# Kernel tuning notes

Measured on AMD Instinct MI355X. Metric: run time of the kernel, lower is better.

## Reference

```python
import math
import jax, jax.numpy as jnp
import numpy as np

B, Q, HID = 4, 4, 4096
NH, NKV, HD = 32, 8, 128
GROUPS = NH // NKV
CACHE_LEN = 4096
CACHE_MAX = CACHE_LEN + 512  # prefill_len + max_len(512)
ROPE_THETA = 500000.0
SCALE = 1.0 / math.sqrt(128.0)  # hardcoded softmax_scale in module


def rotate_half(x):
    x1, x2 = jnp.split(x, 2, axis=-1)
    return jnp.concatenate([-x2, x1], axis=-1)


def setup_inputs() -> dict:
    key = jax.random.key(0)
    ks = jax.random.split(key, 8)
    std = 0.02
    # RoPE angles for positions [CACHE_LEN, CACHE_LEN+Q)
    pos = (CACHE_LEN + jnp.arange(Q)).astype(jnp.float32)
    inv_freq = 1.0 / (ROPE_THETA ** (jnp.arange(0, HD, 2, dtype=jnp.float32) / HD))
    freqs = pos[:, None] * inv_freq[None, :]            # [Q, HD/2]
    emb = jnp.concatenate([freqs, freqs], axis=-1)      # [Q, HD]
    cos = jnp.broadcast_to(jnp.cos(emb)[None], (B, Q, HD)).astype(jnp.float32)
    sin = jnp.broadcast_to(jnp.sin(emb)[None], (B, Q, HD)).astype(jnp.float32)
    return {
        "hidden_states": jax.random.normal(ks[0], (B, Q, HID), jnp.float32),
        "cos": cos,
        "sin": sin,
        "K_Cache": jax.random.normal(ks[1], (B, NKV, CACHE_MAX, HD), jnp.float32) * 0.5,
        "V_Cache": jax.random.normal(ks[2], (B, NKV, CACHE_MAX, HD), jnp.float32) * 0.5,
        "Wq": jax.random.normal(ks[3], (NH * HD, HID), jnp.float32) * std,
        "Wk": jax.random.normal(ks[4], (NKV * HD, HID), jnp.float32) * std,
        "Wv": jax.random.normal(ks[5], (NKV * HD, HID), jnp.float32) * std,
        "Wo": jax.random.normal(ks[6], (HID, NH * HD), jnp.float32) * std,
        "cache_lens": int(CACHE_LEN),
    }


def reference(hidden_states, cos, sin, K_Cache, V_Cache, Wq, Wk, Wv, Wo, cache_lens):
    b, q, _ = hidden_states.shape
    # projections (torch Linear: x @ W.T), reshape to [b, h, q, d]
    qs = jnp.einsum('bsh,oh->bso', hidden_states, Wq).reshape(b, q, NH, HD).transpose(0, 2, 1, 3)
    ks = jnp.einsum('bsh,oh->bso', hidden_states, Wk).reshape(b, q, NKV, HD).transpose(0, 2, 1, 3)
    vs = jnp.einsum('bsh,oh->bso', hidden_states, Wv).reshape(b, q, NKV, HD).transpose(0, 2, 1, 3)
    # RoPE, unsqueeze_dim=1 (head axis)
    c, s = cos[:, None, :, :], sin[:, None, :, :]
    qs = qs * c + rotate_half(qs) * s
    ks = ks * c + rotate_half(ks) * s
    # scatter new K/V into the cache at offset cache_lens
    K_Cache = K_Cache.at[:, :, cache_lens:cache_lens + q, :].set(ks)
    V_Cache = V_Cache.at[:, :, cache_lens:cache_lens + q, :].set(vs)
    # K_total/V_total = cache prefix ++ fresh keys/values; GQA repeat
    K_total = jnp.repeat(jnp.concatenate([K_Cache[:, :, :cache_lens, :], ks], axis=2), GROUPS, axis=1)
    V_total = jnp.repeat(jnp.concatenate([V_Cache[:, :, :cache_lens, :], vs], axis=2), GROUPS, axis=1)
    scores = jnp.einsum('bhqd,bhkd->bhqk', qs, K_total) * SCALE
    # causal mask over the appended q tokens, cache prefix fully visible
    tri = jnp.triu(jnp.ones((q, q), bool), 1)
    mask = jnp.concatenate([jnp.zeros((q, cache_lens), bool), tri], axis=1)
    scores = jnp.where(mask[None, None], -jnp.inf, scores)
    attn = jax.nn.softmax(scores.astype(jnp.float32), axis=-1).astype(V_total.dtype)
    out = jnp.einsum('bhqk,bhkd->bhqd', attn, V_total)
    out = out.transpose(0, 2, 1, 3).reshape(b, q, NH * HD)
    return jnp.einsum('bsh,oh->bso', out, Wo)
```

## Files before the change

### kernel.cpp

```cpp
#include <hip/hip_runtime.h>
#include <hip/hip_fp16.h>
#include <math.h>

#define HIDK 4096
#define NHQ 32
#define HD 128
#define CMAX 4608
#define CLEN 4096
#define NCH 32
#define SCALE 0.08838834764831845f

__device__ __forceinline__ float4 ld4(const float* p) { return *reinterpret_cast<const float4*>(p); }
__device__ __forceinline__ float dot4(float4 a, float4 b) { return a.x*b.x + a.y*b.y + a.z*b.z + a.w*b.w; }

__global__ __launch_bounds__(256) void gemm3_kernel(
    const float* __restrict__ X,
    const float* __restrict__ W1, const float* __restrict__ W2, const float* __restrict__ W3,
    int n1, int n2,
    float* __restrict__ o1, int os1,
    float* __restrict__ o2, int os2,
    float* __restrict__ o3, int os3)
{
  __shared__ float Xs[2][16][256];

  const int tid = threadIdx.x, lane = tid & 63, w = tid >> 6;
  const int o = blockIdx.x * 8 + w * 2;

  const float* Wb; float* ob; int os;
  if (o < n1)           { Wb = W1 + (size_t)o * HIDK;            ob = o1 + o;            os = os1; }
  else if (o < n1 + n2) { const int f = o - n1;      Wb = W2 + (size_t)f * HIDK; ob = o2 + f; os = os2; }
  else                  { const int f = o - n1 - n2; Wb = W3 + (size_t)f * HIDK; ob = o3 + f; os = os3; }

  const int strow = tid >> 6;
  const int stcol = (tid & 63) * 4;

  float acc0[16], acc1[16];
  #pragma unroll
  for (int b = 0; b < 16; ++b) { acc0[b] = 0.f; acc1[b] = 0.f; }

  #pragma unroll
  for (int j = 0; j < 4; ++j)
    *(float4*)&Xs[0][strow + j * 4][stcol] = ld4(X + (size_t)(strow + j * 4) * HIDK + stcol);

  int cur = 0;
  #pragma unroll 2
  for (int kt = 0; kt < 16; ++kt) {
    const float4 w0 = ld4(Wb + (size_t)kt * 256 + lane * 4);
    const float4 w1 = ld4(Wb + HIDK + (size_t)kt * 256 + lane * 4);
    float4 g[4];
    if (kt < 15) {
      #pragma unroll
      for (int j = 0; j < 4; ++j)
        g[j] = ld4(X + (size_t)(strow + j * 4) * HIDK + (kt + 1) * 256 + stcol);
    }
    __syncthreads();
    #pragma unroll
    for (int b = 0; b < 16; ++b) {
      const float4 x4 = *(const float4*)&Xs[cur][b][lane * 4];
      acc0[b] += dot4(x4, w0);
      acc1[b] += dot4(x4, w1);
    }
    if (kt < 15) {
      #pragma unroll
      for (int j = 0; j < 4; ++j)
        *(float4*)&Xs[cur ^ 1][strow + j * 4][stcol] = g[j];
    }
    cur ^= 1;
  }

  #pragma unroll
  for (int m = 1; m < 64; m <<= 1)
    #pragma unroll
    for (int b = 0; b < 16; ++b) {
      acc0[b] += __shfl_xor(acc0[b], m, 64);
      acc1[b] += __shfl_xor(acc1[b], m, 64);
    }
  if (lane == 0) {
    #pragma unroll
    for (int b = 0; b < 16; ++b) {
      ob[(size_t)b * os]     = acc0[b];
      ob[(size_t)b * os + 1] = acc1[b];
    }
  }
}

__global__ __launch_bounds__(256) void qt_prep_kernel(
    const float* __restrict__ qraw, const float* __restrict__ cosp,
    const float* __restrict__ sinp, float* __restrict__ qt)
{
  const int e = blockIdx.x * 256 + threadIdx.x;
  const int r = e & 15;
  const int d = (e >> 4) & 127;
  const int bkv = e >> 11;
  const int b = bkv >> 3, kv = bkv & 7;
  const int s = r & 3, hl = r >> 2;
  const float* qp = qraw + (size_t)(b * 4 + s) * HIDK + (kv * 4 + hl) * HD;
  const float c  = cosp[(b * 4 + s) * HD + d];
  const float sn = sinp[(b * 4 + s) * HD + d];
  const float sgn = (d < 64) ? -1.f : 1.f;
  qt[e] = (qp[d] * c + sgn * qp[d ^ 64] * sn) * SCALE;
}

__global__ __launch_bounds__(128) void attn3_kernel(
    const float* __restrict__ qt, const float* __restrict__ Kc, const float* __restrict__ Vc,
    __half* __restrict__ partOh, float* __restrict__ partM, float* __restrict__ partL)
{
  __shared__ float Plds[2][16][66];
  __shared__ float Oex[16][132];
  __shared__ float MLe[32];

  const int tid = threadIdx.x, lane = tid & 63, w = tid >> 6;
  const int chunk = blockIdx.x & 31, bkv = blockIdx.x >> 5;
  const int b = bkv >> 3, kv = bkv & 7;
  const int p0 = chunk * 128 + w * 64;

  const float* qtb = qt + (size_t)bkv * 2048;
  const float* Kp  = Kc + ((size_t)bkv * CMAX + p0 + lane) * HD;

  float sc[16];
  #pragma unroll
  for (int r = 0; r < 16; ++r) sc[r] = 0.f;
  #pragma unroll 4
  for (int d4 = 0; d4 < 32; ++d4) {
    const float4 k4 = ld4(Kp + d4 * 4);
    #pragma unroll
    for (int r = 0; r < 16; ++r) sc[r] += k4.x * qtb[(d4 * 4 + 0) * 16 + r];
    #pragma unroll
    for (int r = 0; r < 16; ++r) sc[r] += k4.y * qtb[(d4 * 4 + 1) * 16 + r];
    #pragma unroll
    for (int r = 0; r < 16; ++r) sc[r] += k4.z * qtb[(d4 * 4 + 2) * 16 + r];
    #pragma unroll
    for (int r = 0; r < 16; ++r) sc[r] += k4.w * qtb[(d4 * 4 + 3) * 16 + r];
  }

  float m[16], l[16];
  #pragma unroll
  for (int r = 0; r < 16; ++r) {
    float mx = sc[r];
    #pragma unroll
    for (int st = 1; st < 64; st <<= 1) mx = fmaxf(mx, __shfl_xor(mx, st, 64));
    const float p = __expf(sc[r] - mx);
    float ls = p;
    #pragma unroll
    for (int st = 1; st < 64; st <<= 1) ls += __shfl_xor(ls, st, 64);
    m[r] = mx; l[r] = ls;
    Plds[w][r][lane] = p;
  }

  const int dsub = lane & 31, par = lane >> 5;
  const float* Vp = Vc + ((size_t)bkv * CMAX + p0 + par) * HD + dsub * 4;
  float4 o[16];
  #pragma unroll
  for (int r = 0; r < 16; ++r) o[r] = make_float4(0.f, 0.f, 0.f, 0.f);
  #pragma unroll 4
  for (int i = 0; i < 32; ++i) {
    const float4 v4 = ld4(Vp + (size_t)(2 * i) * HD);
    #pragma unroll
    for (int r = 0; r < 16; ++r) {
      const float p = Plds[w][r][2 * i + par];
      o[r].x += p * v4.x; o[r].y += p * v4.y; o[r].z += p * v4.z; o[r].w += p * v4.w;
    }
  }
  #pragma unroll
  for (int r = 0; r < 16; ++r) {
    o[r].x += __shfl_xor(o[r].x, 32, 64);
    o[r].y += __shfl_xor(o[r].y, 32, 64);
    o[r].z += __shfl_xor(o[r].z, 32, 64);
    o[r].w += __shfl_xor(o[r].w, 32, 64);
  }

  if (w == 1) {
    if (lane < 32) {
      #pragma unroll
      for (int r = 0; r < 16; ++r) *(float4*)&Oex[r][dsub * 4] = o[r];
    }
    if (lane == 0) {
      #pragma unroll
      for (int r = 0; r < 16; ++r) { MLe[r] = m[r]; MLe[16 + r] = l[r]; }
    }
  }
  __syncthreads();
  if (w == 0 && lane < 32) {
    #pragma unroll
    for (int r = 0; r < 16; ++r) {
      const float m1 = MLe[r], l1 = MLe[16 + r];
      const float M  = fmaxf(m[r], m1);
      const float a0 = __expf(m[r] - M), a1 = __expf(m1 - M);
      const float4 o1 = *(const float4*)&Oex[r][dsub * 4];
      const float ox = a0 * o[r].x + a1 * o1.x;
      const float oy = a0 * o[r].y + a1 * o1.y;
      const float oz = a0 * o[r].z + a1 * o1.z;
      const float ow = a0 * o[r].w + a1 * o1.w;
      const int row = (b * NHQ + kv * 4 + (r >> 2)) * 4 + (r & 3);
      const size_t idx = ((size_t)row * NCH + chunk) * HD + dsub * 4;
      *(__half2*)&partOh[idx]     = __floats2half2_rn(ox, oy);
      *(__half2*)&partOh[idx + 2] = __floats2half2_rn(oz, ow);
      if (dsub == 0) {
        partM[row * NCH + chunk] = M;
        partL[row * NCH + chunk] = a0 * l[r] + a1 * l1;
      }
    }
  }
}

__global__ __launch_bounds__(64) void combine_kernel(
    const float* __restrict__ qt, const float* __restrict__ kraw, const float* __restrict__ vraw,
    const float* __restrict__ cosp, const float* __restrict__ sinp,
    const __half* __restrict__ partOh, const float* __restrict__ partM, const float* __restrict__ partL,
    float* __restrict__ attn)
{
  const int bid = blockIdx.x;
  const int s = bid & 3;
  const int h = (bid >> 2) & 31;
  const int b = bid >> 7;
  const int kv = h >> 2;
  const int lane = threadIdx.x;
  const int d0 = lane * 2;

  float M = -INFINITY;
  #pragma unroll 4
  for (int c = 0; c < NCH; ++c) M = fmaxf(M, partM[bid * NCH + c]);

  const int rloc = (h & 3) * 4 + s;
  const float qr0 = qt[((size_t)(b * 8 + kv) * 128 + d0) * 16 + rloc];
  const float qr1 = qt[((size_t)(b * 8 + kv) * 128 + d0 + 1) * 16 + rloc];

  float sj[4] = {0.f, 0.f, 0.f, 0.f};
  float Mp = M;
  #pragma unroll
  for (int j = 0; j < 4; ++j) {
    if (j <= s) {
      const float* kp = kraw + (size_t)(b * 4 + j) * 1024 + kv * HD;
      const float c0 = cosp[(b * 4 + j) * HD + d0],     sn0 = sinp[(b * 4 + j) * HD + d0];
      const float c1 = cosp[(b * 4 + j) * HD + d0 + 1], sn1 = sinp[(b * 4 + j) * HD + d0 + 1];
      const float sg0 = (d0 < 64) ? -1.f : 1.f;
      const float sg1 = ((d0 + 1) < 64) ? -1.f : 1.f;
      const float kr0 = kp[d0] * c0 + sg0 * kp[d0 ^ 64] * sn0;
      const float kr1 = kp[d0 + 1] * c1 + sg1 * kp[(d0 + 1) ^ 64] * sn1;
      float part = qr0 * kr0 + qr1 * kr1;
      #pragma unroll
      for (int m = 1; m < 64; m <<= 1) part += __shfl_xor(part, m, 64);
      sj[j] = part;
      Mp = fmaxf(Mp, part);
    }
  }

  float ltot = 0.f, O0 = 0.f, O1 = 0.f;
  #pragma unroll 4
  for (int c = 0; c < NCH; ++c) {
    const float a = __expf(partM[bid * NCH + c] - Mp);
    ltot += partL[bid * NCH + c] * a;
    const float2 v = __half22float2(*(const __half2*)&partOh[((size_t)bid * NCH + c) * HD + d0]);
    O0 += a * v.x;
    O1 += a * v.y;
  }
  #pragma unroll
  for (int j = 0; j < 4; ++j) {
    if (j <= s) {
      const float e = __expf(sj[j] - Mp);
      ltot += e;
      const float* vp = vraw + (size_t)(b * 4 + j) * 1024 + kv * HD + d0;
      O0 += e * vp[0];
      O1 += e * vp[1];
    }
  }
  const float inv = 1.f / ltot;
  *(float2*)&attn[(size_t)(b * 4 + s) * HIDK + h * HD + d0] = make_float2(O0 * inv, O1 * inv);
}

extern "C" void kernel_launch(void* const* d_in, const int* in_sizes, int n_in,
                              void* d_out, int out_size, void* d_ws, size_t ws_size,
                              hipStream_t stream)
{
  const float* hid  = (const float*)d_in[0];
  const float* cosp = (const float*)d_in[1];
  const float* sinp = (const float*)d_in[2];
  const float* Kc   = (const float*)d_in[3];
  const float* Vc   = (const float*)d_in[4];
  const float* Wq   = (const float*)d_in[5];
  const float* Wk   = (const float*)d_in[6];
  const float* Wv   = (const float*)d_in[7];
  const float* Wo   = (const float*)d_in[8];
  float* out = (float*)d_out;

  float* ws    = (float*)d_ws;
  float*  kraw   = ws;
  float*  vraw   = ws + 16384;
  float*  attn   = ws + 32768;
  float*  qt     = ws + 98304;
  float*  qraw   = ws + 163840;
  float*  partM  = ws + 229376;
  float*  partL  = ws + 245760;
  __half* partOh = (__half*)(ws + 262144);

  gemm3_kernel<<<768, 256, 0, stream>>>(hid, Wq, Wk, Wv, 4096, 1024,
                                        qraw, 4096, kraw, 1024, vraw, 1024);
  qt_prep_kernel<<<256, 256, 0, stream>>>(qraw, cosp, sinp, qt);
  attn3_kernel<<<1024, 128, 0, stream>>>(qt, Kc, Vc, partOh, partM, partL);
  combine_kernel<<<512, 64, 0, stream>>>(qt, kraw, vraw, cosp, sinp,
                                         partOh, partM, partL, attn);
  gemm3_kernel<<<512, 256, 0, stream>>>(attn, Wo, Wo, Wo, 4096, 0,
                                        out, 4096, out, 4096, out, 4096);
}
```

Baseline: 121.4 us.

## Rewrite attention split kernel with fp16 dot2 scores and four-wave layout

The attention kernel now runs four waves per block, each handling 32 cache positions with the head dimension split across two half-waves. Q is stored transposed in fp16 in shared memory, and QK scores are computed with packed fp16 dot2 instructions after converting K to fp16. The PV loop software-prefetches V rows, and a four-way partial merge goes through fp16 shared memory. The aim is to cut the ALU cost of the score computation and raise occupancy and memory-level parallelism on the cache-bound attention, at the cost of reduced precision in both the scores and the partial outputs.

```diff
diff --git a/kernel.cpp b/kernel.cpp
--- a/kernel.cpp
+++ b/kernel.cpp
@@ -10,8 +10,22 @@
 #define NCH 32
 #define SCALE 0.08838834764831845f
 
+typedef _Float16 h2 __attribute__((ext_vector_type(2)));
+
 __device__ __forceinline__ float4 ld4(const float* p) { return *reinterpret_cast<const float4*>(p); }
 __device__ __forceinline__ float dot4(float4 a, float4 b) { return a.x*b.x + a.y*b.y + a.z*b.z + a.w*b.w; }
+
+__device__ __forceinline__ h2 pk16(float x, float y) {
+  return __builtin_bit_cast(h2, __builtin_amdgcn_cvt_pkrtz(x, y));
+}
+
+__device__ __forceinline__ float fdot2f(h2 a, h2 b, float c) {
+#if __has_builtin(__builtin_amdgcn_fdot2)
+  return __builtin_amdgcn_fdot2(a, b, c, false);
+#else
+  return c + (float)a.x * (float)b.x + (float)a.y * (float)b.y;
+#endif
+}
 
 __global__ __launch_bounds__(256) void gemm3_kernel(
     const float* __restrict__ X,
@@ -86,11 +100,11 @@
 
 __global__ __launch_bounds__(256) void qt_prep_kernel(
     const float* __restrict__ qraw, const float* __restrict__ cosp,
-    const float* __restrict__ sinp, float* __restrict__ qt)
+    const float* __restrict__ sinp, float* __restrict__ qt, __half* __restrict__ qth)
 {
   const int e = blockIdx.x * 256 + threadIdx.x;
-  const int r = e & 15;
-  const int d = (e >> 4) & 127;
+  const int d = e & 127;
+  const int r = (e >> 7) & 15;
   const int bkv = e >> 11;
   const int b = bkv >> 3, kv = bkv & 7;
   const int s = r & 3, hl = r >> 2;
@@ -98,106 +112,156 @@
   const float c  = cosp[(b * 4 + s) * HD + d];
   const float sn = sinp[(b * 4 + s) * HD + d];
   const float sgn = (d < 64) ? -1.f : 1.f;
-  qt[e] = (qp[d] * c + sgn * qp[d ^ 64] * sn) * SCALE;
-}
-
-__global__ __launch_bounds__(128) void attn3_kernel(
-    const float* __restrict__ qt, const float* __restrict__ Kc, const float* __restrict__ Vc,
+  const float v = (qp[d] * c + sgn * qp[d ^ 64] * sn) * SCALE;
+  qt[e] = v;
+  qth[e] = (__half)v;
+}
+
+__global__ __launch_bounds__(256) void attn8_kernel(
+    const __half* __restrict__ qth, const float* __restrict__ Kc, const float* __restrict__ Vc,
     __half* __restrict__ partOh, float* __restrict__ partM, float* __restrict__ partL)
 {
-  __shared__ float Plds[2][16][66];
-  __shared__ float Oex[16][132];
-  __shared__ float MLe[32];
+  __shared__ __half qsh[16 * 128];
+  __shared__ float  P[4][32][20];
+  __shared__ __half Oex[3 * 16 * 128];
+  __shared__ float  Mex[4][16];
+  __shared__ float  Lex[4][16];
 
   const int tid = threadIdx.x, lane = tid & 63, w = tid >> 6;
   const int chunk = blockIdx.x & 31, bkv = blockIdx.x >> 5;
   const int b = bkv >> 3, kv = bkv & 7;
-  const int p0 = chunk * 128 + w * 64;
-
-  const float* qtb = qt + (size_t)bkv * 2048;
-  const float* Kp  = Kc + ((size_t)bkv * CMAX + p0 + lane) * HD;
+  const int p0 = chunk * 128;
+
+  ((float4*)qsh)[tid] = ((const float4*)(qth + (size_t)bkv * 2048))[tid];
+  __syncthreads();
+
+  const int pq = lane & 31, dh = lane >> 5;
+  const int posg = p0 + w * 32 + pq;
+  const float* Kp = Kc + ((size_t)bkv * CMAX + posg) * HD + dh * 64;
 
   float sc[16];
   #pragma unroll
   for (int r = 0; r < 16; ++r) sc[r] = 0.f;
-  #pragma unroll 4
-  for (int d4 = 0; d4 < 32; ++d4) {
-    const float4 k4 = ld4(Kp + d4 * 4);
-    #pragma unroll
-    for (int r = 0; r < 16; ++r) sc[r] += k4.x * qtb[(d4 * 4 + 0) * 16 + r];
-    #pragma unroll
-    for (int r = 0; r < 16; ++r) sc[r] += k4.y * qtb[(d4 * 4 + 1) * 16 + r];
-    #pragma unroll
-    for (int r = 0; r < 16; ++r) sc[r] += k4.z * qtb[(d4 * 4 + 2) * 16 + r];
-    #pragma unroll
-    for (int r = 0; r < 16; ++r) sc[r] += k4.w * qtb[(d4 * 4 + 3) * 16 + r];
+
+  #pragma unroll
+  for (int hf = 0; hf < 2; ++hf) {
+    float4 kr[8];
+    #pragma unroll
+    for (int j = 0; j < 8; ++j) kr[j] = ld4(Kp + hf * 32 + j * 4);
+    h2 kh[16];
+    #pragma unroll
+    for (int j = 0; j < 8; ++j) {
+      kh[2 * j]     = pk16(kr[j].x, kr[j].y);
+      kh[2 * j + 1] = pk16(kr[j].z, kr[j].w);
+    }
+    #pragma unroll
+    for (int r = 0; r < 16; ++r) {
+      const float4* qrow = (const float4*)&qsh[r * 128 + dh * 64 + hf * 32];
+      float s = sc[r];
+      #pragma unroll
+      for (int g = 0; g < 4; ++g) {
+        float4 q4 = qrow[g];
+        h2 qh[4];
+        __builtin_memcpy(qh, &q4, 16);
+        s = fdot2f(kh[4 * g + 0], qh[0], s);
+        s = fdot2f(kh[4 * g + 1], qh[1], s);
+        s = fdot2f(kh[4 * g + 2], qh[2], s);
+        s = fdot2f(kh[4 * g + 3], qh[3], s);
+      }
+      sc[r] = s;
+    }
   }
 
   float m[16], l[16];
   #pragma unroll
   for (int r = 0; r < 16; ++r) {
+    sc[r] += __shfl_xor(sc[r], 32, 64);
     float mx = sc[r];
     #pragma unroll
-    for (int st = 1; st < 64; st <<= 1) mx = fmaxf(mx, __shfl_xor(mx, st, 64));
+    for (int st = 1; st < 32; st <<= 1) mx = fmaxf(mx, __shfl_xor(mx, st, 64));
     const float p = __expf(sc[r] - mx);
     float ls = p;
     #pragma unroll
-    for (int st = 1; st < 64; st <<= 1) ls += __shfl_xor(ls, st, 64);
+    for (int st = 1; st < 32; st <<= 1) ls += __shfl_xor(ls, st, 64);
     m[r] = mx; l[r] = ls;
-    Plds[w][r][lane] = p;
-  }
-
-  const int dsub = lane & 31, par = lane >> 5;
-  const float* Vp = Vc + ((size_t)bkv * CMAX + p0 + par) * HD + dsub * 4;
-  float4 o[16];
-  #pragma unroll
-  for (int r = 0; r < 16; ++r) o[r] = make_float4(0.f, 0.f, 0.f, 0.f);
-  #pragma unroll 4
+    if (dh == 0) P[w][pq][r] = p;
+  }
+
+  const int dc = lane & 31, rh = lane >> 5;
+  const float* Vp = Vc + ((size_t)bkv * CMAX + p0 + w * 32) * HD + dc * 4;
+
+  float4 o[8];
+  #pragma unroll
+  for (int j = 0; j < 8; ++j) o[j] = make_float4(0.f, 0.f, 0.f, 0.f);
+
+  float4 vb[4];
+  #pragma unroll
+  for (int j = 0; j < 4; ++j) vb[j] = ld4(Vp + (size_t)j * HD);
+
+  #pragma unroll
   for (int i = 0; i < 32; ++i) {
-    const float4 v4 = ld4(Vp + (size_t)(2 * i) * HD);
-    #pragma unroll
-    for (int r = 0; r < 16; ++r) {
-      const float p = Plds[w][r][2 * i + par];
-      o[r].x += p * v4.x; o[r].y += p * v4.y; o[r].z += p * v4.z; o[r].w += p * v4.w;
-    }
-  }
-  #pragma unroll
-  for (int r = 0; r < 16; ++r) {
-    o[r].x += __shfl_xor(o[r].x, 32, 64);
-    o[r].y += __shfl_xor(o[r].y, 32, 64);
-    o[r].z += __shfl_xor(o[r].z, 32, 64);
-    o[r].w += __shfl_xor(o[r].w, 32, 64);
-  }
-
-  if (w == 1) {
-    if (lane < 32) {
-      #pragma unroll
-      for (int r = 0; r < 16; ++r) *(float4*)&Oex[r][dsub * 4] = o[r];
-    }
-    if (lane == 0) {
-      #pragma unroll
-      for (int r = 0; r < 16; ++r) { MLe[r] = m[r]; MLe[16 + r] = l[r]; }
+    const float4 v4 = vb[i & 3];
+    if (i < 28) vb[i & 3] = ld4(Vp + (size_t)(i + 4) * HD);
+    const float4 pa = *(const float4*)&P[w][i][rh * 8];
+    const float4 pb = *(const float4*)&P[w][i][rh * 8 + 4];
+    o[0].x += pa.x * v4.x; o[0].y += pa.x * v4.y; o[0].z += pa.x * v4.z; o[0].w += pa.x * v4.w;
+    o[1].x += pa.y * v4.x; o[1].y += pa.y * v4.y; o[1].z += pa.y * v4.z; o[1].w += pa.y * v4.w;
+    o[2].x += pa.z * v4.x; o[2].y += pa.z * v4.y; o[2].z += pa.z * v4.z; o[2].w += pa.z * v4.w;
+    o[3].x += pa.w * v4.x; o[3].y += pa.w * v4.y; o[3].z += pa.w * v4.z; o[3].w += pa.w * v4.w;
+    o[4].x += pb.x * v4.x; o[4].y += pb.x * v4.y; o[4].z += pb.x * v4.z; o[4].w += pb.x * v4.w;
+    o[5].x += pb.y * v4.x; o[5].y += pb.y * v4.y; o[5].z += pb.y * v4.z; o[5].w += pb.y * v4.w;
+    o[6].x += pb.z * v4.x; o[6].y += pb.z * v4.y; o[6].z += pb.z * v4.z; o[6].w += pb.z * v4.w;
+    o[7].x += pb.w * v4.x; o[7].y += pb.w * v4.y; o[7].z += pb.w * v4.z; o[7].w += pb.w * v4.w;
+  }
+
+  if (lane == 0) {
+    #pragma unroll
+    for (int r = 0; r < 16; ++r) { Mex[w][r] = m[r]; Lex[w][r] = l[r]; }
+  }
+  if (w > 0) {
+    #pragma unroll
+    for (int j = 0; j < 8; ++j) {
+      const int row = rh * 8 + j;
+      __half2* dst = (__half2*)&Oex[((w - 1) * 16 + row) * 128 + dc * 4];
+      dst[0] = __floats2half2_rn(o[j].x, o[j].y);
+      dst[1] = __floats2half2_rn(o[j].z, o[j].w);
     }
   }
   __syncthreads();
-  if (w == 0 && lane < 32) {
-    #pragma unroll
-    for (int r = 0; r < 16; ++r) {
-      const float m1 = MLe[r], l1 = MLe[16 + r];
-      const float M  = fmaxf(m[r], m1);
-      const float a0 = __expf(m[r] - M), a1 = __expf(m1 - M);
-      const float4 o1 = *(const float4*)&Oex[r][dsub * 4];
-      const float ox = a0 * o[r].x + a1 * o1.x;
-      const float oy = a0 * o[r].y + a1 * o1.y;
-      const float oz = a0 * o[r].z + a1 * o1.z;
-      const float ow = a0 * o[r].w + a1 * o1.w;
-      const int row = (b * NHQ + kv * 4 + (r >> 2)) * 4 + (r & 3);
-      const size_t idx = ((size_t)row * NCH + chunk) * HD + dsub * 4;
-      *(__half2*)&partOh[idx]     = __floats2half2_rn(ox, oy);
-      *(__half2*)&partOh[idx + 2] = __floats2half2_rn(oz, ow);
-      if (dsub == 0) {
-        partM[row * NCH + chunk] = M;
-        partL[row * NCH + chunk] = a0 * l[r] + a1 * l1;
+  if (w == 0) {
+    #pragma unroll
+    for (int j = 0; j < 8; ++j) {
+      const int row = rh * 8 + j;
+      const float m0 = Mex[0][row], m1 = Mex[1][row], m2 = Mex[2][row], m3 = Mex[3][row];
+      const float M = fmaxf(fmaxf(m0, m1), fmaxf(m2, m3));
+      const float a0 = __expf(m0 - M), a1 = __expf(m1 - M);
+      const float a2 = __expf(m2 - M), a3 = __expf(m3 - M);
+      float4 O;
+      O.x = a0 * o[j].x; O.y = a0 * o[j].y; O.z = a0 * o[j].z; O.w = a0 * o[j].w;
+      {
+        const __half2* s1 = (const __half2*)&Oex[(0 * 16 + row) * 128 + dc * 4];
+        const float2 x0 = __half22float2(s1[0]), x1 = __half22float2(s1[1]);
+        O.x += a1 * x0.x; O.y += a1 * x0.y; O.z += a1 * x1.x; O.w += a1 * x1.y;
+      }
+      {
+        const __half2* s2 = (const __half2*)&Oex[(1 * 16 + row) * 128 + dc * 4];
+        const float2 x0 = __half22float2(s2[0]), x1 = __half22float2(s2[1]);
+        O.x += a2 * x0.x; O.y += a2 * x0.y; O.z += a2 * x1.x; O.w += a2 * x1.y;
+      }
+      {
+        const __half2* s3 = (const __half2*)&Oex[(2 * 16 + row) * 128 + dc * 4];
+        const float2 x0 = __half22float2(s3[0]), x1 = __half22float2(s3[1]);
+        O.x += a3 * x0.x; O.y += a3 * x0.y; O.z += a3 * x1.x; O.w += a3 * x1.y;
+      }
+      const float lf = a0 * Lex[0][row] + a1 * Lex[1][row] + a2 * Lex[2][row] + a3 * Lex[3][row];
+      const int hl = row >> 2, s = row & 3;
+      const int grow = (b * NHQ + kv * 4 + hl) * 4 + s;
+      const size_t idx = ((size_t)grow * NCH + chunk) * HD + dc * 4;
+      *(__half2*)&partOh[idx]     = __floats2half2_rn(O.x, O.y);
+      *(__half2*)&partOh[idx + 2] = __floats2half2_rn(O.z, O.w);
+      if (dc == 0) {
+        partM[grow * NCH + chunk] = M;
+        partL[grow * NCH + chunk] = lf;
       }
     }
   }
@@ -222,8 +286,8 @@
   for (int c = 0; c < NCH; ++c) M = fmaxf(M, partM[bid * NCH + c]);
 
   const int rloc = (h & 3) * 4 + s;
-  const float qr0 = qt[((size_t)(b * 8 + kv) * 128 + d0) * 16 + rloc];
-  const float qr1 = qt[((size_t)(b * 8 + kv) * 128 + d0 + 1) * 16 + rloc];
+  const float qr0 = qt[((size_t)(b * 8 + kv) * 16 + rloc) * 128 + d0];
+  const float qr1 = qt[((size_t)(b * 8 + kv) * 16 + rloc) * 128 + d0 + 1];
 
   float sj[4] = {0.f, 0.f, 0.f, 0.f};
   float Mp = M;
@@ -288,15 +352,16 @@
   float*  vraw   = ws + 16384;
   float*  attn   = ws + 32768;
   float*  qt     = ws + 98304;
-  float*  qraw   = ws + 163840;
-  float*  partM  = ws + 229376;
-  float*  partL  = ws + 245760;
-  __half* partOh = (__half*)(ws + 262144);
+  __half* qth    = (__half*)(ws + 163840);
+  float*  qraw   = ws + 196608;
+  float*  partM  = ws + 262144;
+  float*  partL  = ws + 278528;
+  __half* partOh = (__half*)(ws + 294912);
 
   gemm3_kernel<<<768, 256, 0, stream>>>(hid, Wq, Wk, Wv, 4096, 1024,
                                         qraw, 4096, kraw, 1024, vraw, 1024);
-  qt_prep_kernel<<<256, 256, 0, stream>>>(qraw, cosp, sinp, qt);
-  attn3_kernel<<<1024, 128, 0, stream>>>(qt, Kc, Vc, partOh, partM, partL);
+  qt_prep_kernel<<<256, 256, 0, stream>>>(qraw, cosp, sinp, qt, qth);
+  attn8_kernel<<<1024, 256, 0, stream>>>(qth, Kc, Vc, partOh, partM, partL);
   combine_kernel<<<512, 64, 0, stream>>>(qt, kraw, vraw, cosp, sinp,
                                          partOh, partM, partL, attn);
   gemm3_kernel<<<512, 256, 0, stream>>>(attn, Wo, Wo, Wo, 4096, 0,
```

Measured after the change: 159.9 us. 31.8% more time.
